# Kernel tuning notes

Hardware: AMD Instinct MI355X
Metric: run time of the kernel (lower is better)

The kernel has to match this reference:

```python
import jax, jax.numpy as jnp
import numpy as np

N, E = 50000, 800000
IN_F, HID, HEADS, OUT_F = 128, 32, 4, 40
SLOPE = 0.2  # LeakyReLU negative slope (alpha)


def gatv2_layer(x, Wl, Wr, att, src, dst, n):
    # GATv2 (Brody et al.): score_ij = att . leakyrelu(Wl x_j + Wr x_i), message = Wl x_j
    H, F = att.shape
    gl = (x @ Wl).reshape(n, H, F)  # [N,H,F] source transform
    gr = (x @ Wr).reshape(n, H, F)  # [N,H,F] dest transform
    s = gl[src] + gr[dst]           # [E,H,F]
    e = jnp.where(s > 0, s, SLOPE * s)
    score = jnp.einsum('ehf,hf->eh', e, att)  # [E,H]
    m = jax.lax.stop_gradient(jax.ops.segment_max(score, dst, num_segments=n))
    a = jnp.exp(score - m[dst])
    denom = jax.ops.segment_sum(a, dst, num_segments=n)  # [N,H]
    w = a / (denom[dst] + 1e-16)                          # softmax over incoming edges
    out = jax.ops.segment_sum(w[:, :, None] * gl[src], dst, num_segments=n)  # [N,H,F]
    return out.reshape(n, H * F)


def setup_inputs() -> dict:
    key = jax.random.key(0)
    ks = jax.random.split(key, 12)
    d1 = HEADS * HID  # 128
    sc_in = 1.0 / np.sqrt(IN_F)
    sc_h = 1.0 / np.sqrt(d1)
    return {
        'x': jax.random.normal(ks[0], (N, IN_F), jnp.float32),
        'Wl1': jax.random.normal(ks[1], (IN_F, d1), jnp.float32) * sc_in,
        'Wr1': jax.random.normal(ks[2], (IN_F, d1), jnp.float32) * sc_in,
        'att1': jax.random.normal(ks[3], (HEADS, HID), jnp.float32) * (1.0 / np.sqrt(HID)),
        'Wl2': jax.random.normal(ks[4], (d1, d1), jnp.float32) * sc_h,
        'Wr2': jax.random.normal(ks[5], (d1, d1), jnp.float32) * sc_h,
        'att2': jax.random.normal(ks[6], (HEADS, HID), jnp.float32) * (1.0 / np.sqrt(HID)),
        'Wl3': jax.random.normal(ks[7], (d1, OUT_F), jnp.float32) * sc_h,
        'Wr3': jax.random.normal(ks[8], (d1, OUT_F), jnp.float32) * sc_h,
        'att3': jax.random.normal(ks[9], (1, OUT_F), jnp.float32) * (1.0 / np.sqrt(OUT_F)),
        'edge_index': jax.random.randint(ks[10], (2, E), 0, N, jnp.int64 if jax.config.jax_enable_x64 else jnp.int32),
    }


def reference(x, Wl1, Wr1, att1, Wl2, Wr2, att2, Wl3, Wr3, att3, edge_index):
    src, dst = edge_index[0], edge_index[1]
    h = jax.nn.elu(gatv2_layer(x, Wl1, Wr1, att1, src, dst, N))        # conv1 + ELU
    h = jax.nn.relu(gatv2_layer(h, Wl2, Wr2, att2, src, dst, N))       # hidden + ReLU (dropout off: eval)
    h = gatv2_layer(h, Wl3, Wr3, att3, src, dst, N)                    # conv2, 1 head
    return jax.nn.log_softmax(h, axis=1)
```

## Files before the change

### kernel.cpp

```cpp
#include <hip/hip_runtime.h>
#include <math.h>


#define TPB 256

typedef __attribute__((ext_vector_type(8))) short short8v;
typedef __attribute__((ext_vector_type(4))) float f32x4;

__device__ __forceinline__ short bf16rne(float v, float* recon) {
  unsigned u = __float_as_uint(v);
  unsigned r = (u + 0x7FFFu + ((u >> 16) & 1u)) >> 16;
  if (recon) *recon = __uint_as_float(r << 16);
  return (short)r;
}
__device__ __forceinline__ float bf2f(unsigned short u) {
  return __uint_as_float((unsigned)u << 16);
}

__global__ void k_prepX(const float* __restrict__ x, unsigned short* __restrict__ ah,
                        unsigned short* __restrict__ al, int total8) {
  int t = blockIdx.x * blockDim.x + threadIdx.x;
  if (t >= total8) return;
  const float4* px = reinterpret_cast<const float4*>(x) + (size_t)t * 2;
  float4 a = px[0], b = px[1];
  float av[8] = {a.x, a.y, a.z, a.w, b.x, b.y, b.z, b.w};
  short8v h, l;
#pragma unroll
  for (int j = 0; j < 8; ++j) {
    float vh;
    h[j] = bf16rne(av[j], &vh);
    l[j] = bf16rne(av[j] - vh, nullptr);
  }
  *reinterpret_cast<short8v*>(ah + (size_t)t * 8) = h;
  *reinterpret_cast<short8v*>(al + (size_t)t * 8) = l;
}

__global__ void k_prepW6(const float* __restrict__ s0, const float* __restrict__ s1,
                         const float* __restrict__ s2, const float* __restrict__ s3,
                         const float* __restrict__ s4, const float* __restrict__ s5,
                         short* __restrict__ wt) {
  int y = blockIdx.y;
  const float* W; short* hi; int M, Mp;
  if (y < 4) {
    W = (y == 0) ? s0 : (y == 1) ? s1 : (y == 2) ? s2 : s3;
    hi = wt + y * 32768; M = 128; Mp = 128;
  } else {
    W = (y == 4) ? s4 : s5;
    hi = wt + 131072 + (y - 4) * 12288; M = 40; Mp = 48;
  }
  short* lo = hi + 128 * Mp;
  int t = blockIdx.x * blockDim.x + threadIdx.x;
  if (t >= 128 * Mp) return;
  int m = t % Mp, k = t / Mp;
  float v = (m < M) ? W[k * M + m] : 0.f;
  float vh;
  short h = bf16rne(v, &vh);
  short l = bf16rne(v - vh, nullptr);
  hi[(size_t)m * 128 + k] = h;
  lo[(size_t)m * 128 + k] = l;
}

__global__ __launch_bounds__(256) void k_gemm_mfma(
    const unsigned short* __restrict__ ah, const unsigned short* __restrict__ al,
    const short* __restrict__ blh, const short* __restrict__ bll,
    const short* __restrict__ brh, const short* __restrict__ brl,
    unsigned short* __restrict__ glh, float* __restrict__ gr, int n) {
  const int K = 128;
  int lane = threadIdx.x & 63;
  int w = threadIdx.x >> 6;
  int rbase = blockIdx.x * 16;
  int arow = rbase + (lane & 15);
  if (arow >= n) arow = n - 1;
  int koff = (lane >> 4) * 8;

  short8v AH[4], AL[4];
#pragma unroll
  for (int k = 0; k < 4; ++k) {
    AH[k] = *reinterpret_cast<const short8v*>(ah + (size_t)arow * 128 + k * 32 + koff);
    AL[k] = *reinterpret_cast<const short8v*>(al + (size_t)arow * 128 + k * 32 + koff);
  }

  f32x4 acc[2][2];
#pragma unroll
  for (int m = 0; m < 2; ++m)
#pragma unroll
    for (int c = 0; c < 2; ++c) acc[m][c] = (f32x4)(0.f);

  int bbase = (lane & 15) * K + koff;
  const int cb = w * 2;

#define BOFF(IT) (((cb + ((IT) & 1)) * 16 * K) + bbase + (((IT) >> 1) * 32))
  short8v cbh = *reinterpret_cast<const short8v*>(blh + BOFF(0));
  short8v cbl = *reinterpret_cast<const short8v*>(bll + BOFF(0));
  short8v cch = *reinterpret_cast<const short8v*>(brh + BOFF(0));
  short8v ccl = *reinterpret_cast<const short8v*>(brl + BOFF(0));
#pragma unroll
  for (int it = 0; it < 8; ++it) {
    const int k0i = it >> 1, ci = it & 1;
    const int nit = (it + 1) & 7;
    short8v nbh = *reinterpret_cast<const short8v*>(blh + BOFF(nit));
    short8v nbl = *reinterpret_cast<const short8v*>(bll + BOFF(nit));
    short8v nch = *reinterpret_cast<const short8v*>(brh + BOFF(nit));
    short8v ncl = *reinterpret_cast<const short8v*>(brl + BOFF(nit));
    acc[0][ci] = __builtin_amdgcn_mfma_f32_16x16x32_bf16(AH[k0i], cbh, acc[0][ci], 0, 0, 0);
    acc[0][ci] = __builtin_amdgcn_mfma_f32_16x16x32_bf16(AH[k0i], cbl, acc[0][ci], 0, 0, 0);
    acc[0][ci] = __builtin_amdgcn_mfma_f32_16x16x32_bf16(AL[k0i], cbh, acc[0][ci], 0, 0, 0);
    acc[1][ci] = __builtin_amdgcn_mfma_f32_16x16x32_bf16(AH[k0i], cch, acc[1][ci], 0, 0, 0);
    acc[1][ci] = __builtin_amdgcn_mfma_f32_16x16x32_bf16(AH[k0i], ccl, acc[1][ci], 0, 0, 0);
    acc[1][ci] = __builtin_amdgcn_mfma_f32_16x16x32_bf16(AL[k0i], cch, acc[1][ci], 0, 0, 0);
    cbh = nbh; cbl = nbl; cch = nch; ccl = ncl;
  }
#undef BOFF

  int crow = rbase + (lane >> 4) * 4;
  int ccol = lane & 15;
#pragma unroll
  for (int ci = 0; ci < 2; ++ci) {
    int c = cb + ci;
#pragma unroll
    for (int j = 0; j < 4; ++j) {
      int r = crow + j;
      if (r < n) {
        glh[(size_t)r * 128 + c * 16 + ccol] = (unsigned short)bf16rne(acc[0][ci][j], nullptr);
        gr[(size_t)r * 128 + c * 16 + ccol] = acc[1][ci][j];
      }
    }
  }
}

__global__ __launch_bounds__(192) void k_gemm_mfma3(
    const unsigned short* __restrict__ ah, const unsigned short* __restrict__ al,
    const short* __restrict__ blh, const short* __restrict__ bll,
    const short* __restrict__ brh, const short* __restrict__ brl,
    unsigned short* __restrict__ glh, float* __restrict__ gr, int n) {
  const int K = 128;
  int lane = threadIdx.x & 63;
  int w = threadIdx.x >> 6;
  int rbase = blockIdx.x * 16;
  int arow = rbase + (lane & 15);
  if (arow >= n) arow = n - 1;
  int koff = (lane >> 4) * 8;

  short8v AH[4], AL[4];
#pragma unroll
  for (int k = 0; k < 4; ++k) {
    AH[k] = *reinterpret_cast<const short8v*>(ah + (size_t)arow * 128 + k * 32 + koff);
    AL[k] = *reinterpret_cast<const short8v*>(al + (size_t)arow * 128 + k * 32 + koff);
  }

  int bbase = w * 16 * K + (lane & 15) * K + koff;

  short8v Bh[4], Bl[4], Ch[4], Cl[4];
#pragma unroll
  for (int k = 0; k < 4; ++k) {
    Bh[k] = *reinterpret_cast<const short8v*>(blh + bbase + k * 32);
    Bl[k] = *reinterpret_cast<const short8v*>(bll + bbase + k * 32);
    Ch[k] = *reinterpret_cast<const short8v*>(brh + bbase + k * 32);
    Cl[k] = *reinterpret_cast<const short8v*>(brl + bbase + k * 32);
  }

  f32x4 accL = (f32x4)(0.f), accR = (f32x4)(0.f);
#pragma unroll
  for (int k = 0; k < 4; ++k) {
    accL = __builtin_amdgcn_mfma_f32_16x16x32_bf16(AH[k], Bh[k], accL, 0, 0, 0);
    accL = __builtin_amdgcn_mfma_f32_16x16x32_bf16(AH[k], Bl[k], accL, 0, 0, 0);
    accL = __builtin_amdgcn_mfma_f32_16x16x32_bf16(AL[k], Bh[k], accL, 0, 0, 0);
    accR = __builtin_amdgcn_mfma_f32_16x16x32_bf16(AH[k], Ch[k], accR, 0, 0, 0);
    accR = __builtin_amdgcn_mfma_f32_16x16x32_bf16(AH[k], Cl[k], accR, 0, 0, 0);
    accR = __builtin_amdgcn_mfma_f32_16x16x32_bf16(AL[k], Ch[k], accR, 0, 0, 0);
  }

  int crow = rbase + (lane >> 4) * 4;
  int ccol = lane & 15;
  int col = w * 16 + ccol;
#pragma unroll
  for (int j = 0; j < 4; ++j) {
    int r = crow + j;
    if (r < n && col < 40) {
      glh[(size_t)r * 40 + col] = (unsigned short)bf16rne(accL[j], nullptr);
      gr[(size_t)r * 40 + col] = accR[j];
    }
  }
}

__global__ void k_hist(const int* __restrict__ dst, int* __restrict__ cnt, int E) {
  int e = blockIdx.x * blockDim.x + threadIdx.x;
  if (e < E) atomicAdd(&cnt[dst[e]], 1);
}

__global__ void k_scan1(const int* __restrict__ cnt, int* __restrict__ rowptr,
                        int* __restrict__ bsum, int n) {
  __shared__ int wsum[16];
  int i = blockIdx.x * 1024 + threadIdx.x;
  int lane = threadIdx.x & 63, wid = threadIdx.x >> 6;
  int v = (i < n) ? cnt[i] : 0;
  int x = v;
#pragma unroll
  for (int off = 1; off < 64; off <<= 1) {
    int t = __shfl_up(x, off);
    if (lane >= off) x += t;
  }
  if (lane == 63) wsum[wid] = x;
  __syncthreads();
  if (wid == 0) {
    int wv = (lane < 16) ? wsum[lane] : 0;
#pragma unroll
    for (int off = 1; off < 16; off <<= 1) {
      int t = __shfl_up(wv, off);
      if (lane >= off) wv += t;
    }
    if (lane < 16) wsum[lane] = wv;
  }
  __syncthreads();
  int woff = wid ? wsum[wid - 1] : 0;
  if (i < n) rowptr[i] = woff + x - v;
  if (threadIdx.x == 1023) bsum[blockIdx.x] = wsum[15];
}

__global__ void k_scan2(const int* __restrict__ bsum, int* __restrict__ boff, int nb,
                        int* __restrict__ rowptr, int n) {
  int lane = threadIdx.x;
  int v = (lane < nb) ? bsum[lane] : 0;
  int x = v;
#pragma unroll
  for (int off = 1; off < 64; off <<= 1) {
    int t = __shfl_up(x, off);
    if (lane >= off) x += t;
  }
  if (lane < nb) boff[lane] = x - v;
  if (lane == 63) rowptr[n] = x;
}

__global__ void k_scan3(int* __restrict__ rowptr, const int* __restrict__ boff,
                        int* __restrict__ cur, int n) {
  int i = blockIdx.x * blockDim.x + threadIdx.x;
  if (i < n) {
    int r = rowptr[i] + boff[i >> 10];
    rowptr[i] = r;
    cur[i] = r;
  }
}

__global__ void k_fill(const int* __restrict__ src, const int* __restrict__ dst,
                       int* __restrict__ cur, int* __restrict__ csr_src, int E) {
  int e = blockIdx.x * blockDim.x + threadIdx.x;
  if (e >= E) return;
  int pos = atomicAdd(&cur[dst[e]], 1);
  csr_src[pos] = src[e];
}

template <int ACTOUT>
__global__ void k_edge4(const unsigned short* __restrict__ glh, const float* __restrict__ gr,
                        const float* __restrict__ att, const int* __restrict__ rowptr,
                        const int* __restrict__ csr_src,
                        unsigned short* __restrict__ oah, unsigned short* __restrict__ oal,
                        int n) {
  int wid = (int)((blockIdx.x * blockDim.x + threadIdx.x) >> 6);
  if (wid >= n) return;
  int lane = threadIdx.x & 63;
  int p0 = rowptr[wid], p1 = rowptr[wid + 1];
  ushort2* pah = reinterpret_cast<ushort2*>(oah + (size_t)wid * 128) + lane;
  ushort2* pal = reinterpret_cast<ushort2*>(oal + (size_t)wid * 128) + lane;
  if (p1 <= p0) { *pah = make_ushort2(0, 0); *pal = make_ushort2(0, 0); return; }
  const float2 grv = reinterpret_cast<const float2*>(gr + (size_t)wid * 128)[lane];
  const float2 attv = reinterpret_cast<const float2*>(att)[lane];

  float l[8];
  float2 acc[8];
#pragma unroll
  for (int j = 0; j < 8; ++j) { l[j] = 0.f; acc[j] = make_float2(0.f, 0.f); }

#define LD(S) ({ ushort2 u_ = reinterpret_cast<const ushort2*>(glh + ((size_t)(S) << 7))[lane]; \
                 make_float2(bf2f(u_.x), bf2f(u_.y)); })
#define UPD4(J, G)                                                     \
  {                                                                    \
    float vx = (G).x + grv.x; vx = vx > 0.f ? vx : 0.2f * vx;          \
    float vy = (G).y + grv.y; vy = vy > 0.f ? vy : 0.2f * vy;          \
    float part = fmaf(vx, attv.x, vy * attv.y);                        \
    part += __shfl_xor(part, 1);                                       \
    part += __shfl_xor(part, 2);                                       \
    part += __shfl_xor(part, 4);                                       \
    part += __shfl_xor(part, 8);                                       \
    float w = __expf(part);                                            \
    l[J] += w;                                                         \
    acc[J].x = fmaf(w, (G).x, acc[J].x);                               \
    acc[J].y = fmaf(w, (G).y, acc[J].y);                               \
  }

  for (int base = p0; base < p1; base += 64) {
    int nv = p1 - base; if (nv > 64) nv = 64;
    int sv = (base + lane < p1) ? csr_src[base + lane] : 0;
    int i = 0;
    for (; i + 8 <= nv; i += 8) {
      int s0 = __shfl(sv, i + 0), s1 = __shfl(sv, i + 1);
      int s2 = __shfl(sv, i + 2), s3 = __shfl(sv, i + 3);
      int s4 = __shfl(sv, i + 4), s5 = __shfl(sv, i + 5);
      int s6 = __shfl(sv, i + 6), s7 = __shfl(sv, i + 7);
      float2 g0 = LD(s0), g1 = LD(s1), g2 = LD(s2), g3 = LD(s3);
      float2 g4 = LD(s4), g5 = LD(s5), g6 = LD(s6), g7 = LD(s7);
      UPD4(0, g0); UPD4(1, g1); UPD4(2, g2); UPD4(3, g3);
      UPD4(4, g4); UPD4(5, g5); UPD4(6, g6); UPD4(7, g7);
    }
    for (; i < nv; ++i) {
      int s0 = __shfl(sv, i);
      float2 g0 = LD(s0);
      UPD4(0, g0);
    }
  }
#undef UPD4
#undef LD

  float lt = 0.f;
  float2 at = make_float2(0.f, 0.f);
#pragma unroll
  for (int j = 0; j < 8; ++j) {
    lt += l[j];
    at.x += acc[j].x;
    at.y += acc[j].y;
  }
  float inv = 1.f / (lt + 1e-16f);
  float ox = at.x * inv, oy = at.y * inv;
  if (ACTOUT == 1) {
    ox = ox > 0.f ? ox : (__expf(ox) - 1.f);
    oy = oy > 0.f ? oy : (__expf(oy) - 1.f);
  } else {
    ox = fmaxf(ox, 0.f);
    oy = fmaxf(oy, 0.f);
  }
  float rx, ry;
  unsigned short hx = (unsigned short)bf16rne(ox, &rx);
  unsigned short hy = (unsigned short)bf16rne(oy, &ry);
  unsigned short lx = (unsigned short)bf16rne(ox - rx, nullptr);
  unsigned short ly = (unsigned short)bf16rne(oy - ry, nullptr);
  *pah = make_ushort2(hx, hy);
  *pal = make_ushort2(lx, ly);
}

__global__ void k_edge1ls(const unsigned short* __restrict__ glh, const float* __restrict__ gr,
                          const float* __restrict__ att, const int* __restrict__ rowptr,
                          const int* __restrict__ csr_src, float* __restrict__ outf, int n) {
  int wv = (int)((blockIdx.x * blockDim.x + threadIdx.x) >> 6);
  int lane = threadIdx.x & 63;
  int half = lane >> 5, hl = lane & 31;
  int d = wv * 2 + half;
  if (d >= n) d = n - 1;
  bool fok = hl < 20;
  float2 grv = fok ? reinterpret_cast<const float2*>(gr + (size_t)d * 40)[hl]
                   : make_float2(0.f, 0.f);
  float2 attv = fok ? reinterpret_cast<const float2*>(att)[hl] : make_float2(0.f, 0.f);
  int p0 = rowptr[d], p1 = rowptr[d + 1];
  int ec = p1 - p0;
  int nch = (ec + 31) >> 5;
  { int o = __shfl_xor(nch, 32); nch = nch > o ? nch : o; }

  float l0 = 0.f, l1 = 0.f;
  float2 a0 = make_float2(0.f, 0.f), a1 = make_float2(0.f, 0.f);

  for (int c = 0; c < nch; ++c) {
    int base = p0 + c * 32;
    int sv = (base + hl < p1) ? csr_src[base + hl] : 0;
    int nv = p1 - base;
    nv = nv < 0 ? 0 : (nv > 32 ? 32 : nv);
    int nvmax = nv;
    { int o = __shfl_xor(nvmax, 32); nvmax = nvmax > o ? nvmax : o; }
    for (int i = 0; i < nvmax; i += 2) {
      int s0 = __shfl(sv, (half << 5) + i);
      int s1 = __shfl(sv, (half << 5) + i + 1);
      bool v0 = i < nv, v1 = (i + 1) < nv;
      float2 g0 = make_float2(0.f, 0.f), g1 = make_float2(0.f, 0.f);
      if (v0 && fok) { ushort2 u = reinterpret_cast<const ushort2*>(glh + (size_t)s0 * 40)[hl]; g0 = make_float2(bf2f(u.x), bf2f(u.y)); }
      if (v1 && fok) { ushort2 u = reinterpret_cast<const ushort2*>(glh + (size_t)s1 * 40)[hl]; g1 = make_float2(bf2f(u.x), bf2f(u.y)); }
      float e0x = g0.x + grv.x; e0x = e0x > 0.f ? e0x : 0.2f * e0x;
      float e0y = g0.y + grv.y; e0y = e0y > 0.f ? e0y : 0.2f * e0y;
      float pt0 = fmaf(e0x, attv.x, e0y * attv.y);
      float e1x = g1.x + grv.x; e1x = e1x > 0.f ? e1x : 0.2f * e1x;
      float e1y = g1.y + grv.y; e1y = e1y > 0.f ? e1y : 0.2f * e1y;
      float pt1 = fmaf(e1x, attv.x, e1y * attv.y);
#pragma unroll
      for (int o = 1; o < 32; o <<= 1) {
        pt0 += __shfl_xor(pt0, o);
        pt1 += __shfl_xor(pt1, o);
      }
      float w0 = v0 ? __expf(pt0) : 0.f;
      float w1 = v1 ? __expf(pt1) : 0.f;
      l0 += w0;
      a0.x = fmaf(w0, g0.x, a0.x);
      a0.y = fmaf(w0, g0.y, a0.y);
      l1 += w1;
      a1.x = fmaf(w1, g1.x, a1.x);
      a1.y = fmaf(w1, g1.y, a1.y);
    }
  }

  float lt = l0 + l1;
  float inv = 1.f / (lt + 1e-16f);
  float ox = (a0.x + a1.x) * inv;
  float oy = (a0.y + a1.y) * inv;

  float mx = fok ? fmaxf(ox, oy) : -INFINITY;
#pragma unroll
  for (int o = 1; o < 32; o <<= 1) mx = fmaxf(mx, __shfl_xor(mx, o));
  float ex = fok ? (__expf(ox - mx) + __expf(oy - mx)) : 0.f;
  float sm = ex;
#pragma unroll
  for (int o = 1; o < 32; o <<= 1) sm += __shfl_xor(sm, o);
  float lg = logf(sm);
  if (fok) {
    float2* po = reinterpret_cast<float2*>(outf + (size_t)d * 40);
    po[hl] = make_float2(ox - mx - lg, oy - mx - lg);
  }
}

static inline int cdiv(long long a, int b) { return (int)((a + b - 1) / b); }

extern "C" void kernel_launch(void* const* d_in, const int* in_sizes, int n_in,
                              void* d_out, int out_size, void* d_ws, size_t ws_size,
                              hipStream_t stream) {
  const float* x    = (const float*)d_in[0];
  const float* Wl1  = (const float*)d_in[1];
  const float* Wr1  = (const float*)d_in[2];
  const float* att1 = (const float*)d_in[3];
  const float* Wl2  = (const float*)d_in[4];
  const float* Wr2  = (const float*)d_in[5];
  const float* att2 = (const float*)d_in[6];
  const float* Wl3  = (const float*)d_in[7];
  const float* Wr3  = (const float*)d_in[8];
  const float* att3 = (const float*)d_in[9];
  const int*   ei   = (const int*)d_in[10];

  const int N = in_sizes[0] / 128;
  const int E = in_sizes[10] / 2;
  const int* src = ei;
  const int* dst = ei + E;

  short* wt = (short*)d_ws;
  short* wl1h = wt +      0;  short* wl1l = wt +  16384;
  short* wr1h = wt +  32768;  short* wr1l = wt +  49152;
  short* wl2h = wt +  65536;  short* wl2l = wt +  81920;
  short* wr2h = wt +  98304;  short* wr2l = wt + 114688;
  short* wl3h = wt + 131072;  short* wl3l = wt + 137216;
  short* wr3h = wt + 143360;  short* wr3l = wt + 149504;

  unsigned short* ah  = (unsigned short*)(wt + 155648);
  unsigned short* al  = ah + (size_t)N * 128;
  float* bufGR        = (float*)(al + (size_t)N * 128);
  unsigned short* glh = (unsigned short*)(bufGR + (size_t)N * 128);
  int*   cnt    = (int*)(glh + (size_t)N * 128);
  int*   rowptr = cnt + N;
  int*   cur    = rowptr + N + 1;
  int*   csrS   = cur + N;
  int*   bsum   = csrS + E;
  int*   boff   = bsum + 64;

  float* outf = (float*)d_out;

  const int nb = cdiv(N, 1024);

  hipMemsetAsync(cnt, 0, (size_t)N * sizeof(int), stream);
  k_hist<<<cdiv(E, TPB), TPB, 0, stream>>>(dst, cnt, E);
  k_prepW6<<<dim3(64, 6), TPB, 0, stream>>>(Wl1, Wr1, Wl2, Wr2, Wl3, Wr3, wt);
  k_prepX<<<cdiv((long long)N * 16, TPB), TPB, 0, stream>>>(x, ah, al, N * 16);
  k_scan1<<<nb, 1024, 0, stream>>>(cnt, rowptr, bsum, N);
  k_scan2<<<1, 64, 0, stream>>>(bsum, boff, nb, rowptr, N);
  k_scan3<<<cdiv(N, TPB), TPB, 0, stream>>>(rowptr, boff, cur, N);
  k_fill<<<cdiv(E, TPB), TPB, 0, stream>>>(src, dst, cur, csrS, E);

  k_gemm_mfma<<<cdiv(N, 16), 256, 0, stream>>>(ah, al, wl1h, wl1l, wr1h, wr1l, glh, bufGR, N);
  k_edge4<1><<<cdiv(N, 4), TPB, 0, stream>>>(glh, bufGR, att1, rowptr, csrS, ah, al, N);

  k_gemm_mfma<<<cdiv(N, 16), 256, 0, stream>>>(ah, al, wl2h, wl2l, wr2h, wr2l, glh, bufGR, N);
  k_edge4<2><<<cdiv(N, 4), TPB, 0, stream>>>(glh, bufGR, att2, rowptr, csrS, ah, al, N);

  k_gemm_mfma3<<<cdiv(N, 16), 192, 0, stream>>>(ah, al, wl3h, wl3l, wr3h, wr3l, glh, bufGR, N);
  k_edge1ls<<<cdiv(cdiv(N, 2), 4), TPB, 0, stream>>>(glh, bufGR, att3, rowptr, csrS, outf, N);
}
```

Before: 509.7 us.

## Stage 64-row A tiles in LDS and keep B fragments in registers for GEMMs

Replaces the two GEMM kernels with one templated kernel. Each block loads a 64-row tile of the split-bf16 activations into padded LDS, keeps each wave's 16-column slice of the weight fragments in registers, and loops over four 16-row subtiles. The old kernels reloaded weight fragments from global memory for every 16 rows, and this aims to cut that traffic. In exchange it adds about 35 KB of LDS per block plus a barrier, and uses 512-thread blocks for the 128-wide layers, which may lower occupancy.

```diff
diff --git a/kernel.cpp b/kernel.cpp
--- a/kernel.cpp
+++ b/kernel.cpp
@@ -60,96 +60,21 @@
   lo[(size_t)m * 128 + k] = l;
 }
 
-__global__ __launch_bounds__(256) void k_gemm_mfma(
+template <int NCG, int MOUT>
+__global__ __launch_bounds__(NCG * 64) void k_gemm_lds(
     const unsigned short* __restrict__ ah, const unsigned short* __restrict__ al,
     const short* __restrict__ blh, const short* __restrict__ bll,
     const short* __restrict__ brh, const short* __restrict__ brl,
     unsigned short* __restrict__ glh, float* __restrict__ gr, int n) {
   const int K = 128;
+  __shared__ unsigned short aldsH[64][136];
+  __shared__ unsigned short aldsL[64][136];
+
   int lane = threadIdx.x & 63;
   int w = threadIdx.x >> 6;
-  int rbase = blockIdx.x * 16;
-  int arow = rbase + (lane & 15);
-  if (arow >= n) arow = n - 1;
-  int koff = (lane >> 4) * 8;
-
-  short8v AH[4], AL[4];
-#pragma unroll
-  for (int k = 0; k < 4; ++k) {
-    AH[k] = *reinterpret_cast<const short8v*>(ah + (size_t)arow * 128 + k * 32 + koff);
-    AL[k] = *reinterpret_cast<const short8v*>(al + (size_t)arow * 128 + k * 32 + koff);
-  }
-
-  f32x4 acc[2][2];
-#pragma unroll
-  for (int m = 0; m < 2; ++m)
-#pragma unroll
-    for (int c = 0; c < 2; ++c) acc[m][c] = (f32x4)(0.f);
-
-  int bbase = (lane & 15) * K + koff;
-  const int cb = w * 2;
-
-#define BOFF(IT) (((cb + ((IT) & 1)) * 16 * K) + bbase + (((IT) >> 1) * 32))
-  short8v cbh = *reinterpret_cast<const short8v*>(blh + BOFF(0));
-  short8v cbl = *reinterpret_cast<const short8v*>(bll + BOFF(0));
-  short8v cch = *reinterpret_cast<const short8v*>(brh + BOFF(0));
-  short8v ccl = *reinterpret_cast<const short8v*>(brl + BOFF(0));
-#pragma unroll
-  for (int it = 0; it < 8; ++it) {
-    const int k0i = it >> 1, ci = it & 1;
-    const int nit = (it + 1) & 7;
-    short8v nbh = *reinterpret_cast<const short8v*>(blh + BOFF(nit));
-    short8v nbl = *reinterpret_cast<const short8v*>(bll + BOFF(nit));
-    short8v nch = *reinterpret_cast<const short8v*>(brh + BOFF(nit));
-    short8v ncl = *reinterpret_cast<const short8v*>(brl + BOFF(nit));
-    acc[0][ci] = __builtin_amdgcn_mfma_f32_16x16x32_bf16(AH[k0i], cbh, acc[0][ci], 0, 0, 0);
-    acc[0][ci] = __builtin_amdgcn_mfma_f32_16x16x32_bf16(AH[k0i], cbl, acc[0][ci], 0, 0, 0);
-    acc[0][ci] = __builtin_amdgcn_mfma_f32_16x16x32_bf16(AL[k0i], cbh, acc[0][ci], 0, 0, 0);
-    acc[1][ci] = __builtin_amdgcn_mfma_f32_16x16x32_bf16(AH[k0i], cch, acc[1][ci], 0, 0, 0);
-    acc[1][ci] = __builtin_amdgcn_mfma_f32_16x16x32_bf16(AH[k0i], ccl, acc[1][ci], 0, 0, 0);
-    acc[1][ci] = __builtin_amdgcn_mfma_f32_16x16x32_bf16(AL[k0i], cch, acc[1][ci], 0, 0, 0);
-    cbh = nbh; cbl = nbl; cch = nch; ccl = ncl;
-  }
-#undef BOFF
-
-  int crow = rbase + (lane >> 4) * 4;
-  int ccol = lane & 15;
-#pragma unroll
-  for (int ci = 0; ci < 2; ++ci) {
-    int c = cb + ci;
-#pragma unroll
-    for (int j = 0; j < 4; ++j) {
-      int r = crow + j;
-      if (r < n) {
-        glh[(size_t)r * 128 + c * 16 + ccol] = (unsigned short)bf16rne(acc[0][ci][j], nullptr);
-        gr[(size_t)r * 128 + c * 16 + ccol] = acc[1][ci][j];
-      }
-    }
-  }
-}
-
-__global__ __launch_bounds__(192) void k_gemm_mfma3(
-    const unsigned short* __restrict__ ah, const unsigned short* __restrict__ al,
-    const short* __restrict__ blh, const short* __restrict__ bll,
-    const short* __restrict__ brh, const short* __restrict__ brl,
-    unsigned short* __restrict__ glh, float* __restrict__ gr, int n) {
-  const int K = 128;
-  int lane = threadIdx.x & 63;
-  int w = threadIdx.x >> 6;
-  int rbase = blockIdx.x * 16;
-  int arow = rbase + (lane & 15);
-  if (arow >= n) arow = n - 1;
-  int koff = (lane >> 4) * 8;
-
-  short8v AH[4], AL[4];
-#pragma unroll
-  for (int k = 0; k < 4; ++k) {
-    AH[k] = *reinterpret_cast<const short8v*>(ah + (size_t)arow * 128 + k * 32 + koff);
-    AL[k] = *reinterpret_cast<const short8v*>(al + (size_t)arow * 128 + k * 32 + koff);
-  }
-
-  int bbase = w * 16 * K + (lane & 15) * K + koff;
-
+  int rbase = blockIdx.x * 64;
+
+  int bbase = (w * 16 + (lane & 15)) * K + (lane >> 4) * 8;
   short8v Bh[4], Bl[4], Ch[4], Cl[4];
 #pragma unroll
   for (int k = 0; k < 4; ++k) {
@@ -159,26 +84,45 @@
     Cl[k] = *reinterpret_cast<const short8v*>(brl + bbase + k * 32);
   }
 
-  f32x4 accL = (f32x4)(0.f), accR = (f32x4)(0.f);
-#pragma unroll
-  for (int k = 0; k < 4; ++k) {
-    accL = __builtin_amdgcn_mfma_f32_16x16x32_bf16(AH[k], Bh[k], accL, 0, 0, 0);
-    accL = __builtin_amdgcn_mfma_f32_16x16x32_bf16(AH[k], Bl[k], accL, 0, 0, 0);
-    accL = __builtin_amdgcn_mfma_f32_16x16x32_bf16(AL[k], Bh[k], accL, 0, 0, 0);
-    accR = __builtin_amdgcn_mfma_f32_16x16x32_bf16(AH[k], Ch[k], accR, 0, 0, 0);
-    accR = __builtin_amdgcn_mfma_f32_16x16x32_bf16(AH[k], Cl[k], accR, 0, 0, 0);
-    accR = __builtin_amdgcn_mfma_f32_16x16x32_bf16(AL[k], Ch[k], accR, 0, 0, 0);
-  }
-
-  int crow = rbase + (lane >> 4) * 4;
+  for (int c = threadIdx.x; c < 64 * 16; c += NCG * 64) {
+    int row = c >> 4, seg = c & 15;
+    int grow = rbase + row;
+    if (grow >= n) grow = n - 1;
+    short8v hv = *reinterpret_cast<const short8v*>(ah + (size_t)grow * 128 + seg * 8);
+    short8v lv = *reinterpret_cast<const short8v*>(al + (size_t)grow * 128 + seg * 8);
+    *reinterpret_cast<short8v*>(&aldsH[row][seg * 8]) = hv;
+    *reinterpret_cast<short8v*>(&aldsL[row][seg * 8]) = lv;
+  }
+  __syncthreads();
+
+  int arow_l = lane & 15;
+  int kb = (lane >> 4) * 8;
   int ccol = lane & 15;
   int col = w * 16 + ccol;
-#pragma unroll
-  for (int j = 0; j < 4; ++j) {
-    int r = crow + j;
-    if (r < n && col < 40) {
-      glh[(size_t)r * 40 + col] = (unsigned short)bf16rne(accL[j], nullptr);
-      gr[(size_t)r * 40 + col] = accR[j];
+
+#pragma unroll
+  for (int t = 0; t < 4; ++t) {
+    int r0 = t * 16 + arow_l;
+    f32x4 accL = (f32x4)(0.f), accR = (f32x4)(0.f);
+#pragma unroll
+    for (int k = 0; k < 4; ++k) {
+      short8v AHf = *reinterpret_cast<const short8v*>(&aldsH[r0][k * 32 + kb]);
+      short8v ALf = *reinterpret_cast<const short8v*>(&aldsL[r0][k * 32 + kb]);
+      accL = __builtin_amdgcn_mfma_f32_16x16x32_bf16(AHf, Bh[k], accL, 0, 0, 0);
+      accL = __builtin_amdgcn_mfma_f32_16x16x32_bf16(AHf, Bl[k], accL, 0, 0, 0);
+      accL = __builtin_amdgcn_mfma_f32_16x16x32_bf16(ALf, Bh[k], accL, 0, 0, 0);
+      accR = __builtin_amdgcn_mfma_f32_16x16x32_bf16(AHf, Ch[k], accR, 0, 0, 0);
+      accR = __builtin_amdgcn_mfma_f32_16x16x32_bf16(AHf, Cl[k], accR, 0, 0, 0);
+      accR = __builtin_amdgcn_mfma_f32_16x16x32_bf16(ALf, Ch[k], accR, 0, 0, 0);
+    }
+    int crow = rbase + t * 16 + (lane >> 4) * 4;
+#pragma unroll
+    for (int j = 0; j < 4; ++j) {
+      int r = crow + j;
+      if (r < n && col < MOUT) {
+        glh[(size_t)r * MOUT + col] = (unsigned short)bf16rne(accL[j], nullptr);
+        gr[(size_t)r * MOUT + col] = accR[j];
+      }
     }
   }
 }
@@ -465,12 +409,12 @@
   k_scan3<<<cdiv(N, TPB), TPB, 0, stream>>>(rowptr, boff, cur, N);
   k_fill<<<cdiv(E, TPB), TPB, 0, stream>>>(src, dst, cur, csrS, E);
 
-  k_gemm_mfma<<<cdiv(N, 16), 256, 0, stream>>>(ah, al, wl1h, wl1l, wr1h, wr1l, glh, bufGR, N);
+  k_gemm_lds<8, 128><<<cdiv(N, 64), 512, 0, stream>>>(ah, al, wl1h, wl1l, wr1h, wr1l, glh, bufGR, N);
   k_edge4<1><<<cdiv(N, 4), TPB, 0, stream>>>(glh, bufGR, att1, rowptr, csrS, ah, al, N);
 
-  k_gemm_mfma<<<cdiv(N, 16), 256, 0, stream>>>(ah, al, wl2h, wl2l, wr2h, wr2l, glh, bufGR, N);
+  k_gemm_lds<8, 128><<<cdiv(N, 64), 512, 0, stream>>>(ah, al, wl2h, wl2l, wr2h, wr2l, glh, bufGR, N);
   k_edge4<2><<<cdiv(N, 4), TPB, 0, stream>>>(glh, bufGR, att2, rowptr, csrS, ah, al, N);
 
-  k_gemm_mfma3<<<cdiv(N, 16), 192, 0, stream>>>(ah, al, wl3h, wl3l, wr3h, wr3l, glh, bufGR, N);
+  k_gemm_lds<3, 40><<<cdiv(N, 64), 192, 0, stream>>>(ah, al, wl3h, wl3l, wr3h, wr3l, glh, bufGR, N);
   k_edge1ls<<<cdiv(cdiv(N, 2), 4), TPB, 0, stream>>>(glh, bufGR, att3, rowptr, csrS, outf, N);
 }
```

Result: faster. 418.3 us (-17.9%).
